# Performance work log

Measured on AMD Instinct MI355X. Metric: run time of the kernel, lower is better.

The kernel has to match this reference:

```python
import jax, jax.numpy as jnp
import numpy as np

DIM = 1024
HEADS = 16
DIM_HEAD = 64
INNER = HEADS * DIM_HEAD
LN_EPS = 1e-5


def setup_inputs() -> dict:
    key = jax.random.key(0)
    ks = jax.random.split(key, 6)
    b, n = 2, 2048
    x = jax.random.normal(ks[0], (b, n, DIM), dtype=jnp.float32)
    attn_bias = jax.random.normal(ks[1], (HEADS, n, n), dtype=jnp.float32)
    # learned params
    ln_gamma = jnp.ones((DIM,), dtype=jnp.float32)
    ln_beta = jnp.zeros((DIM,), dtype=jnp.float32)
    w_qkv = jax.random.normal(ks[2], (DIM, 3 * INNER), dtype=jnp.float32) / np.sqrt(DIM)
    w_out = jax.random.normal(ks[3], (INNER, DIM), dtype=jnp.float32) / np.sqrt(INNER)
    return {"x": x, "attn_bias": attn_bias, "ln_gamma": ln_gamma,
            "ln_beta": ln_beta, "w_qkv": w_qkv, "w_out": w_out}


def reference(x, attn_bias, ln_gamma, ln_beta, w_qkv, w_out):
    b, n, _ = x.shape
    scale = DIM_HEAD ** -0.5
    # LayerNorm
    mu = jnp.mean(x, axis=-1, keepdims=True)
    var = jnp.mean(jnp.square(x - mu), axis=-1, keepdims=True)
    xn = (x - mu) * jax.lax.rsqrt(var + LN_EPS) * ln_gamma + ln_beta
    # QKV projection: [b, n, 3*inner]
    qkv = xn @ w_qkv
    q, k, v = jnp.split(qkv, 3, axis=-1)
    # [b, n, inner] -> [b, h, n, d]
    split_heads = lambda t: t.reshape(b, n, HEADS, DIM_HEAD).transpose(0, 2, 1, 3)
    q, k, v = split_heads(q) * scale, split_heads(k), split_heads(v)
    sim = jnp.einsum('bhid,bhjd->bhij', q, k)
    sim = sim + attn_bias[None]  # broadcast over batch
    mask_value = -jnp.finfo(sim.dtype).max
    causal = jnp.triu(jnp.ones((n, n), dtype=bool), k=1)
    sim = jnp.where(causal, mask_value, sim)
    attn = jax.nn.softmax(sim, axis=-1)
    out = jnp.einsum('bhij,bhjd->bhid', attn, v)
    out = out.transpose(0, 2, 1, 3).reshape(b, n, INNER)
    return out @ w_out
```

## Files before the change

### kernel.cpp

```cpp
#include <hip/hip_runtime.h>
#include <hip/hip_bf16.h>
#include <math.h>

typedef unsigned short u16;
typedef __attribute__((ext_vector_type(8))) __bf16 bf16x8;
typedef __attribute__((ext_vector_type(4))) float f32x4;

static __device__ __forceinline__ u16 f2bf(float f) {
    unsigned int u = __builtin_bit_cast(unsigned int, f);
    u += 0x7fffu + ((u >> 16) & 1u);
    return (u16)(u >> 16);
}

__global__ __launch_bounds__(256) void ln_kernel(
    const float* __restrict__ x, const float* __restrict__ g,
    const float* __restrict__ bta, u16* __restrict__ xn)
{
    const int row = blockIdx.x;
    const int tid = threadIdx.x;
    const float4 v = *(const float4*)&x[(size_t)row * 1024 + tid * 4];
    float s  = v.x + v.y + v.z + v.w;
    float s2 = v.x * v.x + v.y * v.y + v.z * v.z + v.w * v.w;
    #pragma unroll
    for (int off = 32; off; off >>= 1) {
        s  += __shfl_xor(s,  off);
        s2 += __shfl_xor(s2, off);
    }
    __shared__ float red[8];
    if ((tid & 63) == 0) { red[tid >> 6] = s; red[4 + (tid >> 6)] = s2; }
    __syncthreads();
    s  = red[0] + red[1] + red[2] + red[3];
    s2 = red[4] + red[5] + red[6] + red[7];
    const float mean = s * (1.0f / 1024.0f);
    const float var  = s2 * (1.0f / 1024.0f) - mean * mean;
    const float rstd = rsqrtf(var + 1e-5f);
    const float4 gg = *(const float4*)&g[tid * 4];
    const float4 bb = *(const float4*)&bta[tid * 4];
    ushort4 o;
    o.x = f2bf((v.x - mean) * rstd * gg.x + bb.x);
    o.y = f2bf((v.y - mean) * rstd * gg.y + bb.y);
    o.z = f2bf((v.z - mean) * rstd * gg.z + bb.z);
    o.w = f2bf((v.w - mean) * rstd * gg.w + bb.w);
    *(ushort4*)&xn[(size_t)row * 1024 + tid * 4] = o;
}

__global__ __launch_bounds__(256) void transpose_w(
    const float* __restrict__ in, u16* __restrict__ outT, int K, int N)
{
    const int k0 = blockIdx.x * 64, n0 = blockIdx.y * 64;
    const int tid = threadIdx.x;
    __shared__ u16 tile[64][72];
    #pragma unroll
    for (int i = 0; i < 4; ++i) {
        int c = tid + i * 256;
        int kr = c >> 4, nc = (c & 15) * 4;
        float4 v = *(const float4*)&in[(size_t)(k0 + kr) * N + n0 + nc];
        tile[nc + 0][kr] = f2bf(v.x);
        tile[nc + 1][kr] = f2bf(v.y);
        tile[nc + 2][kr] = f2bf(v.z);
        tile[nc + 3][kr] = f2bf(v.w);
    }
    __syncthreads();
    #pragma unroll
    for (int i = 0; i < 4; ++i) {
        int c = tid + i * 256;
        int nr = c >> 4, kc = (c & 15) * 4;
        ushort4 w = *(const ushort4*)&tile[nr][kc];
        *(ushort4*)&outT[(size_t)(n0 + nr) * K + k0 + kc] = w;
    }
}

__global__ __launch_bounds__(256) void transpose_v_kernel(
    const u16* __restrict__ V, u16* __restrict__ Vt)
{
    const int bh = blockIdx.y;
    const int n0 = blockIdx.x * 64;
    const int tid = threadIdx.x;
    __shared__ u16 t[64][72];
    #pragma unroll
    for (int i = 0; i < 2; ++i) {
        int c = tid + (i << 8);
        int nr = c >> 3, dc = (c & 7) * 8;
        int4 v4 = *(const int4*)&V[((size_t)bh * 2048 + n0 + nr) * 64 + dc];
        union { int4 v; u16 u[8]; } uu; uu.v = v4;
        #pragma unroll
        for (int j = 0; j < 8; ++j) t[dc + j][nr] = uu.u[j];
    }
    __syncthreads();
    #pragma unroll
    for (int i = 0; i < 2; ++i) {
        int c = tid + (i << 8);
        int d = c >> 3, nn = (c & 7) * 8;
        int4 v4 = *(const int4*)&t[d][nn];
        *(int4*)&Vt[((size_t)bh * 64 + d) * 2048 + n0 + nn] = v4;
    }
}

template <int EPI>
__global__ __launch_bounds__(256) void gemm_bf16_k(
    const u16* __restrict__ A, const u16* __restrict__ Bt,
    int M, int N, int K,
    float* __restrict__ Cf,
    u16* __restrict__ Qo, u16* __restrict__ Ko, u16* __restrict__ Vo)
{
    __shared__ u16 lds[2][8192];
    const int tid = threadIdx.x;
    const int lane = tid & 63, w = tid >> 6;
    const int l15 = lane & 15, l4 = lane >> 4;
    const int wm = w & 1, wn = w >> 1;
    const int n0 = blockIdx.x * 128, m0 = blockIdx.y * 128;

    auto stage = [&](int buf, int kt) {
        const u16* Ab = A + (size_t)m0 * K + kt * 32;
        const u16* Bb = Bt + (size_t)n0 * K + kt * 32;
        #pragma unroll
        for (int i = 0; i < 2; ++i) {
            int c = tid + (i << 8);
            int r = c >> 2, ke = (c & 3) * 8;
            __builtin_amdgcn_global_load_lds(
                (const __attribute__((address_space(1))) void*)(Ab + (size_t)r * K + ke),
                (__attribute__((address_space(3))) void*)(&lds[buf][0] + c * 8), 16, 0, 0);
            __builtin_amdgcn_global_load_lds(
                (const __attribute__((address_space(1))) void*)(Bb + (size_t)r * K + ke),
                (__attribute__((address_space(3))) void*)(&lds[buf][4096] + c * 8), 16, 0, 0);
        }
    };

    f32x4 acc[4][4];
    #pragma unroll
    for (int mf = 0; mf < 4; ++mf)
        #pragma unroll
        for (int nf = 0; nf < 4; ++nf)
            acc[mf][nf] = f32x4{0.f, 0.f, 0.f, 0.f};

    const int NT = K >> 5;
    stage(0, 0);
    __syncthreads();
    for (int kt = 0; kt < NT; ++kt) {
        const int buf = kt & 1;
        if (kt + 1 < NT) stage(buf ^ 1, kt + 1);
        const u16* Ab = &lds[buf][0];
        const u16* Bb = &lds[buf][4096];
        bf16x8 af[4], bfv[4];
        #pragma unroll
        for (int mf = 0; mf < 4; ++mf)
            af[mf] = *(const bf16x8*)(Ab + (wm * 64 + mf * 16 + l15) * 32 + l4 * 8);
        #pragma unroll
        for (int nf = 0; nf < 4; ++nf)
            bfv[nf] = *(const bf16x8*)(Bb + (wn * 64 + nf * 16 + l15) * 32 + l4 * 8);
        #pragma unroll
        for (int mf = 0; mf < 4; ++mf)
            #pragma unroll
            for (int nf = 0; nf < 4; ++nf)
                acc[mf][nf] = __builtin_amdgcn_mfma_f32_16x16x32_bf16(
                    af[mf], bfv[nf], acc[mf][nf], 0, 0, 0);
        __syncthreads();
    }

    #pragma unroll
    for (int mf = 0; mf < 4; ++mf) {
        #pragma unroll
        for (int nf = 0; nf < 4; ++nf) {
            #pragma unroll
            for (int r = 0; r < 4; ++r) {
                const int row = m0 + wm * 64 + mf * 16 + l4 * 4 + r;
                const int col = n0 + wn * 64 + nf * 16 + l15;
                const float v = acc[mf][nf][r];
                if (EPI == 1) {
                    Cf[(size_t)row * N + col] = v;
                } else {
                    const int t = col >> 10, rem = col & 1023;
                    const int h = rem >> 6, d = rem & 63;
                    const int b = row >> 11, nn = row & 2047;
                    const size_t idx = ((size_t)((b * 16 + h) * 2048 + nn)) * 64 + d;
                    if (t == 0)      Qo[idx] = f2bf(v * 0.125f);
                    else if (t == 1) Ko[idx] = f2bf(v);
                    else             Vo[idx] = f2bf(v);
                }
            }
        }
    }
}

__global__ __launch_bounds__(512, 4) void attn_kernel(
    const u16* __restrict__ Q, const u16* __restrict__ Kmat,
    const u16* __restrict__ Vt, const float* __restrict__ bias,
    u16* __restrict__ att)
{
    const int hb = blockIdx.x;
    const int h = hb >> 1, b = hb & 1;
    const int bh = b * 16 + h;
    const int y = blockIdx.y;
    const int qb = (y < 8) ? y : 23 - y;
    const int q0 = qb << 7;
    const int tid = threadIdx.x;
    const int w = tid >> 6, lane = tid & 63;
    const int l15 = lane & 15, l4 = lane >> 4;

    __shared__ u16 K_lds[2][64][72];
    __shared__ u16 V_lds[2][64][72];
    __shared__ u16 P_lds[8][16][72];

    const int qrow_a = q0 + w * 16 + l15;
    bf16x8 qa[2];
    #pragma unroll
    for (int ks = 0; ks < 2; ++ks)
        qa[ks] = *(const bf16x8*)(Q + ((size_t)bh * 2048 + qrow_a) * 64 + ks * 32 + l4 * 8);

    f32x4 acc_o[4];
    #pragma unroll
    for (int nf = 0; nf < 4; ++nf) acc_o[nf] = f32x4{0.f, 0.f, 0.f, 0.f};
    float m_r[4], l_r[4];
    #pragma unroll
    for (int r = 0; r < 4; ++r) { m_r[r] = -INFINITY; l_r[r] = 0.f; }

    const int qrow_c = q0 + w * 16 + l4 * 4;
    const float* biasrow = bias + (size_t)h * 2048 * 2048;

    const int rr_s = tid >> 3, pp_s = (tid & 7) * 8;
    int4 kreg, vreg;
    auto issue_loads = [&](int j0n) {
        kreg = *(const int4*)&Kmat[((size_t)bh * 2048 + j0n + rr_s) * 64 + pp_s];
        vreg = *(const int4*)&Vt[((size_t)bh * 64 + rr_s) * 2048 + j0n + pp_s];
    };
    issue_loads(0);

    const int NT = 2 * qb + 2;
    for (int jt = 0; jt < NT; ++jt) {
        const int j0 = jt << 6;
        const int buf = jt & 1;
        *(int4*)&K_lds[buf][rr_s][pp_s] = kreg;
        *(int4*)&V_lds[buf][rr_s][pp_s] = vreg;
        if (jt + 1 < NT) issue_loads(j0 + 64);
        float breg[4][4];
        #pragma unroll
        for (int nf = 0; nf < 4; ++nf)
            #pragma unroll
            for (int r = 0; r < 4; ++r)
                breg[nf][r] = biasrow[(size_t)(qrow_c + r) * 2048 + j0 + nf * 16 + l15];
        __syncthreads();

        f32x4 s[4];
        #pragma unroll
        for (int nf = 0; nf < 4; ++nf) s[nf] = f32x4{0.f, 0.f, 0.f, 0.f};
        __builtin_amdgcn_s_setprio(1);
        #pragma unroll
        for (int ks = 0; ks < 2; ++ks)
            #pragma unroll
            for (int nf = 0; nf < 4; ++nf) {
                bf16x8 kb = *(const bf16x8*)&K_lds[buf][nf * 16 + l15][ks * 32 + l4 * 8];
                s[nf] = __builtin_amdgcn_mfma_f32_16x16x32_bf16(qa[ks], kb, s[nf], 0, 0, 0);
            }
        __builtin_amdgcn_s_setprio(0);

        float sv[4][4];
        if (j0 + 63 > q0 + w * 16) {
            #pragma unroll
            for (int nf = 0; nf < 4; ++nf) {
                const int col = j0 + nf * 16 + l15;
                #pragma unroll
                for (int r = 0; r < 4; ++r) {
                    const int qr = qrow_c + r;
                    float v = s[nf][r] + breg[nf][r];
                    sv[nf][r] = (col > qr) ? -1e30f : v;
                }
            }
        } else {
            #pragma unroll
            for (int nf = 0; nf < 4; ++nf)
                #pragma unroll
                for (int r = 0; r < 4; ++r)
                    sv[nf][r] = s[nf][r] + breg[nf][r];
        }
        float mt[4];
        #pragma unroll
        for (int r = 0; r < 4; ++r)
            mt[r] = fmaxf(fmaxf(sv[0][r], sv[1][r]), fmaxf(sv[2][r], sv[3][r]));
        #pragma unroll
        for (int off = 1; off < 16; off <<= 1)
            #pragma unroll
            for (int r = 0; r < 4; ++r) mt[r] = fmaxf(mt[r], __shfl_xor(mt[r], off));
        float alpha[4];
        #pragma unroll
        for (int r = 0; r < 4; ++r) {
            const float mn = fmaxf(m_r[r], mt[r]);
            alpha[r] = __expf(m_r[r] - mn);
            m_r[r] = mn;
        }
        float pv[4][4], ps[4] = {0.f, 0.f, 0.f, 0.f};
        #pragma unroll
        for (int nf = 0; nf < 4; ++nf)
            #pragma unroll
            for (int r = 0; r < 4; ++r) {
                const float p = __expf(sv[nf][r] - m_r[r]);
                pv[nf][r] = p;
                ps[r] += p;
            }
        #pragma unroll
        for (int off = 1; off < 16; off <<= 1)
            #pragma unroll
            for (int r = 0; r < 4; ++r) ps[r] += __shfl_xor(ps[r], off);
        #pragma unroll
        for (int r = 0; r < 4; ++r) l_r[r] = l_r[r] * alpha[r] + ps[r];
        #pragma unroll
        for (int nf = 0; nf < 4; ++nf)
            #pragma unroll
            for (int r = 0; r < 4; ++r) acc_o[nf][r] *= alpha[r];

        #pragma unroll
        for (int nf = 0; nf < 4; ++nf)
            #pragma unroll
            for (int r = 0; r < 4; ++r)
                P_lds[w][l4 * 4 + r][nf * 16 + l15] = f2bf(pv[nf][r]);

        __builtin_amdgcn_s_setprio(1);
        #pragma unroll
        for (int ks = 0; ks < 2; ++ks) {
            bf16x8 pa = *(const bf16x8*)&P_lds[w][l15][ks * 32 + l4 * 8];
            #pragma unroll
            for (int nf = 0; nf < 4; ++nf) {
                bf16x8 vb = *(const bf16x8*)&V_lds[buf][nf * 16 + l15][ks * 32 + l4 * 8];
                acc_o[nf] = __builtin_amdgcn_mfma_f32_16x16x32_bf16(pa, vb, acc_o[nf], 0, 0, 0);
            }
        }
        __builtin_amdgcn_s_setprio(0);
    }

    #pragma unroll
    for (int nf = 0; nf < 4; ++nf)
        #pragma unroll
        for (int r = 0; r < 4; ++r) {
            const int qr = qrow_c + r;
            const float o = acc_o[nf][r] / l_r[r];
            att[((size_t)b * 2048 + qr) * 1024 + h * 64 + nf * 16 + l15] = f2bf(o);
        }
}

extern "C" void kernel_launch(void* const* d_in, const int* in_sizes, int n_in,
                              void* d_out, int out_size, void* d_ws, size_t ws_size,
                              hipStream_t stream) {
    const float* x     = (const float*)d_in[0];
    const float* bias  = (const float*)d_in[1];
    const float* gamma = (const float*)d_in[2];
    const float* beta_ = (const float*)d_in[3];
    const float* wqkv  = (const float*)d_in[4];
    const float* wout  = (const float*)d_in[5];
    float* out = (float*)d_out;

    char* ws = (char*)d_ws;
    u16* xn     = (u16*)(ws + 0);
    u16* wqkvT  = (u16*)(ws + 8388608);
    u16* woutT  = (u16*)(ws + 14680064);
    u16* Qb     = (u16*)(ws + 16777216);
    u16* Kb     = (u16*)(ws + 25165824);
    u16* Vb     = (u16*)(ws + 33554432);
    u16* Vtb    = (u16*)(ws + 41943040);
    u16* attb   = xn;

    ln_kernel<<<4096, 256, 0, stream>>>(x, gamma, beta_, xn);
    transpose_w<<<dim3(16, 48), 256, 0, stream>>>(wqkv, wqkvT, 1024, 3072);
    transpose_w<<<dim3(16, 16), 256, 0, stream>>>(wout, woutT, 1024, 1024);
    gemm_bf16_k<0><<<dim3(24, 32), 256, 0, stream>>>(xn, wqkvT, 4096, 3072, 1024,
                                                     nullptr, Qb, Kb, Vb);
    transpose_v_kernel<<<dim3(32, 32), 256, 0, stream>>>(Vb, Vtb);
    attn_kernel<<<dim3(32, 16), 512, 0, stream>>>(Qb, Kb, Vtb, bias, attb);
    gemm_bf16_k<1><<<dim3(8, 32), 256, 0, stream>>>(attb, woutT, 4096, 1024, 1024,
                                                    out, nullptr, nullptr, nullptr);
}
```

Before: 154.7 us.

## Process two KV tiles per barrier, load V directly, lazy softmax rescale

Restructures the attention main loop to stage two 64-wide K tiles per sync into a 4-deep K LDS buffer. V fragments are no longer staged in LDS and are read straight from global memory per tile. Whole tiles beyond a wave's causal bound are skipped per wave. The online-softmax rescale now runs only when some row max grows by more than 8, which removes the max shuffles and exp rescaling on most tiles but lets unnormalized exponentials reach up to e^8 before the bf16 cast. Direct global V loads add per-tile memory latency that the pre-MFMA softmax work must hide.

```diff
diff --git a/kernel.cpp b/kernel.cpp
--- a/kernel.cpp
+++ b/kernel.cpp
@@ -197,8 +197,7 @@
     const int w = tid >> 6, lane = tid & 63;
     const int l15 = lane & 15, l4 = lane >> 4;
 
-    __shared__ u16 K_lds[2][64][72];
-    __shared__ u16 V_lds[2][64][72];
+    __shared__ u16 K_lds[4][64][72];
     __shared__ u16 P_lds[8][16][72];
 
     const int qrow_a = q0 + w * 16 + l15;
@@ -216,114 +215,138 @@
 
     const int qrow_c = q0 + w * 16 + l4 * 4;
     const float* biasrow = bias + (size_t)h * 2048 * 2048;
+    const u16* vbase = Vt + (size_t)bh * 64 * 2048;
+    const u16* kbase = Kmat + (size_t)bh * 2048 * 64;
 
     const int rr_s = tid >> 3, pp_s = (tid & 7) * 8;
-    int4 kreg, vreg;
-    auto issue_loads = [&](int j0n) {
-        kreg = *(const int4*)&Kmat[((size_t)bh * 2048 + j0n + rr_s) * 64 + pp_s];
-        vreg = *(const int4*)&Vt[((size_t)bh * 64 + rr_s) * 2048 + j0n + pp_s];
-    };
-    issue_loads(0);
-
-    const int NT = 2 * qb + 2;
-    for (int jt = 0; jt < NT; ++jt) {
-        const int j0 = jt << 6;
-        const int buf = jt & 1;
-        *(int4*)&K_lds[buf][rr_s][pp_s] = kreg;
-        *(int4*)&V_lds[buf][rr_s][pp_s] = vreg;
-        if (jt + 1 < NT) issue_loads(j0 + 64);
-        float breg[4][4];
-        #pragma unroll
-        for (int nf = 0; nf < 4; ++nf)
+    int4 kreg[2];
+    kreg[0] = *(const int4*)&kbase[(size_t)(0 + rr_s) * 64 + pp_s];
+    kreg[1] = *(const int4*)&kbase[(size_t)(64 + rr_s) * 64 + pp_s];
+
+    const int NP = qb + 1;
+    for (int p = 0; p < NP; ++p) {
+        const int base = (p & 1) << 1;
+        *(int4*)&K_lds[base + 0][rr_s][pp_s] = kreg[0];
+        *(int4*)&K_lds[base + 1][rr_s][pp_s] = kreg[1];
+        if (p + 1 < NP) {
+            kreg[0] = *(const int4*)&kbase[(size_t)((2 * p + 2) * 64 + rr_s) * 64 + pp_s];
+            kreg[1] = *(const int4*)&kbase[(size_t)((2 * p + 3) * 64 + rr_s) * 64 + pp_s];
+        }
+        float breg[2][4][4];
+        #pragma unroll
+        for (int t = 0; t < 2; ++t)
+            #pragma unroll
+            for (int nf = 0; nf < 4; ++nf)
+                #pragma unroll
+                for (int r = 0; r < 4; ++r)
+                    breg[t][nf][r] = biasrow[(size_t)(qrow_c + r) * 2048 +
+                                             ((2 * p + t) << 6) + nf * 16 + l15];
+        __syncthreads();
+
+        #pragma unroll
+        for (int t = 0; t < 2; ++t) {
+            const int jt = 2 * p + t;
+            const int j0 = jt << 6;
+            if (j0 > q0 + w * 16 + 15) continue;
+            const int buf = base + t;
+
+            f32x4 s[4];
+            #pragma unroll
+            for (int nf = 0; nf < 4; ++nf) s[nf] = f32x4{0.f, 0.f, 0.f, 0.f};
+            __builtin_amdgcn_s_setprio(1);
+            #pragma unroll
+            for (int ks = 0; ks < 2; ++ks)
+                #pragma unroll
+                for (int nf = 0; nf < 4; ++nf) {
+                    bf16x8 kb = *(const bf16x8*)&K_lds[buf][nf * 16 + l15][ks * 32 + l4 * 8];
+                    s[nf] = __builtin_amdgcn_mfma_f32_16x16x32_bf16(qa[ks], kb, s[nf], 0, 0, 0);
+                }
+            __builtin_amdgcn_s_setprio(0);
+
+            bf16x8 vb[2][4];
+            #pragma unroll
+            for (int ks = 0; ks < 2; ++ks)
+                #pragma unroll
+                for (int nf = 0; nf < 4; ++nf)
+                    vb[ks][nf] = *(const bf16x8*)&vbase[(size_t)(nf * 16 + l15) * 2048 +
+                                                        j0 + ks * 32 + l4 * 8];
+
+            float sv[4][4];
+            if (j0 + 63 > q0 + w * 16) {
+                #pragma unroll
+                for (int nf = 0; nf < 4; ++nf) {
+                    const int col = j0 + nf * 16 + l15;
+                    #pragma unroll
+                    for (int r = 0; r < 4; ++r) {
+                        const int qr = qrow_c + r;
+                        float v = s[nf][r] + breg[t][nf][r];
+                        sv[nf][r] = (col > qr) ? -1e30f : v;
+                    }
+                }
+            } else {
+                #pragma unroll
+                for (int nf = 0; nf < 4; ++nf)
+                    #pragma unroll
+                    for (int r = 0; r < 4; ++r)
+                        sv[nf][r] = s[nf][r] + breg[t][nf][r];
+            }
+
+            float mt[4];
             #pragma unroll
             for (int r = 0; r < 4; ++r)
-                breg[nf][r] = biasrow[(size_t)(qrow_c + r) * 2048 + j0 + nf * 16 + l15];
-        __syncthreads();
-
-        f32x4 s[4];
-        #pragma unroll
-        for (int nf = 0; nf < 4; ++nf) s[nf] = f32x4{0.f, 0.f, 0.f, 0.f};
-        __builtin_amdgcn_s_setprio(1);
-        #pragma unroll
-        for (int ks = 0; ks < 2; ++ks)
-            #pragma unroll
-            for (int nf = 0; nf < 4; ++nf) {
-                bf16x8 kb = *(const bf16x8*)&K_lds[buf][nf * 16 + l15][ks * 32 + l4 * 8];
-                s[nf] = __builtin_amdgcn_mfma_f32_16x16x32_bf16(qa[ks], kb, s[nf], 0, 0, 0);
+                mt[r] = fmaxf(fmaxf(sv[0][r], sv[1][r]), fmaxf(sv[2][r], sv[3][r]));
+            int need = 0;
+            #pragma unroll
+            for (int r = 0; r < 4; ++r) need |= (mt[r] > m_r[r] + 8.0f);
+            if (__any(need)) {
+                #pragma unroll
+                for (int off = 1; off < 16; off <<= 1)
+                    #pragma unroll
+                    for (int r = 0; r < 4; ++r) mt[r] = fmaxf(mt[r], __shfl_xor(mt[r], off));
+                #pragma unroll
+                for (int r = 0; r < 4; ++r) {
+                    const float mn = fmaxf(m_r[r], mt[r]);
+                    const float alpha = __expf(m_r[r] - mn);
+                    m_r[r] = mn;
+                    l_r[r] *= alpha;
+                    #pragma unroll
+                    for (int nf = 0; nf < 4; ++nf) acc_o[nf][r] *= alpha;
+                }
             }
-        __builtin_amdgcn_s_setprio(0);
-
-        float sv[4][4];
-        if (j0 + 63 > q0 + w * 16) {
-            #pragma unroll
-            for (int nf = 0; nf < 4; ++nf) {
-                const int col = j0 + nf * 16 + l15;
+
+            float pv_[4][4], ps[4] = {0.f, 0.f, 0.f, 0.f};
+            #pragma unroll
+            for (int nf = 0; nf < 4; ++nf)
                 #pragma unroll
                 for (int r = 0; r < 4; ++r) {
-                    const int qr = qrow_c + r;
-                    float v = s[nf][r] + breg[nf][r];
-                    sv[nf][r] = (col > qr) ? -1e30f : v;
-                }
+                    const float pp = __expf(sv[nf][r] - m_r[r]);
+                    pv_[nf][r] = pp;
+                    ps[r] += pp;
+                }
+            #pragma unroll
+            for (int off = 1; off < 16; off <<= 1)
+                #pragma unroll
+                for (int r = 0; r < 4; ++r) ps[r] += __shfl_xor(ps[r], off);
+            #pragma unroll
+            for (int r = 0; r < 4; ++r) l_r[r] += ps[r];
+
+            #pragma unroll
+            for (int nf = 0; nf < 4; ++nf)
+                #pragma unroll
+                for (int r = 0; r < 4; ++r)
+                    P_lds[w][l4 * 4 + r][nf * 16 + l15] = f2bf(pv_[nf][r]);
+
+            __builtin_amdgcn_s_setprio(1);
+            #pragma unroll
+            for (int ks = 0; ks < 2; ++ks) {
+                bf16x8 pa = *(const bf16x8*)&P_lds[w][l15][ks * 32 + l4 * 8];
+                #pragma unroll
+                for (int nf = 0; nf < 4; ++nf)
+                    acc_o[nf] = __builtin_amdgcn_mfma_f32_16x16x32_bf16(pa, vb[ks][nf],
+                                                                        acc_o[nf], 0, 0, 0);
             }
-        } else {
-            #pragma unroll
-            for (int nf = 0; nf < 4; ++nf)
-                #pragma unroll
-                for (int r = 0; r < 4; ++r)
-                    sv[nf][r] = s[nf][r] + breg[nf][r];
-        }
-        float mt[4];
-        #pragma unroll
-        for (int r = 0; r < 4; ++r)
-            mt[r] = fmaxf(fmaxf(sv[0][r], sv[1][r]), fmaxf(sv[2][r], sv[3][r]));
-        #pragma unroll
-        for (int off = 1; off < 16; off <<= 1)
-            #pragma unroll
-            for (int r = 0; r < 4; ++r) mt[r] = fmaxf(mt[r], __shfl_xor(mt[r], off));
-        float alpha[4];
-        #pragma unroll
-        for (int r = 0; r < 4; ++r) {
-            const float mn = fmaxf(m_r[r], mt[r]);
-            alpha[r] = __expf(m_r[r] - mn);
-            m_r[r] = mn;
-        }
-        float pv[4][4], ps[4] = {0.f, 0.f, 0.f, 0.f};
-        #pragma unroll
-        for (int nf = 0; nf < 4; ++nf)
-            #pragma unroll
-            for (int r = 0; r < 4; ++r) {
-                const float p = __expf(sv[nf][r] - m_r[r]);
-                pv[nf][r] = p;
-                ps[r] += p;
-            }
-        #pragma unroll
-        for (int off = 1; off < 16; off <<= 1)
-            #pragma unroll
-            for (int r = 0; r < 4; ++r) ps[r] += __shfl_xor(ps[r], off);
-        #pragma unroll
-        for (int r = 0; r < 4; ++r) l_r[r] = l_r[r] * alpha[r] + ps[r];
-        #pragma unroll
-        for (int nf = 0; nf < 4; ++nf)
-            #pragma unroll
-            for (int r = 0; r < 4; ++r) acc_o[nf][r] *= alpha[r];
-
-        #pragma unroll
-        for (int nf = 0; nf < 4; ++nf)
-            #pragma unroll
-            for (int r = 0; r < 4; ++r)
-                P_lds[w][l4 * 4 + r][nf * 16 + l15] = f2bf(pv[nf][r]);
-
-        __builtin_amdgcn_s_setprio(1);
-        #pragma unroll
-        for (int ks = 0; ks < 2; ++ks) {
-            bf16x8 pa = *(const bf16x8*)&P_lds[w][l15][ks * 32 + l4 * 8];
-            #pragma unroll
-            for (int nf = 0; nf < 4; ++nf) {
-                bf16x8 vb = *(const bf16x8*)&V_lds[buf][nf * 16 + l15][ks * 32 + l4 * 8];
-                acc_o[nf] = __builtin_amdgcn_mfma_f32_16x16x32_bf16(pa, vb, acc_o[nf], 0, 0, 0);
-            }
-        }
-        __builtin_amdgcn_s_setprio(0);
+            __builtin_amdgcn_s_setprio(0);
+        }
     }
 
     #pragma unroll
```

Result: slower. 296.9 us (+91.9%).
